# Optimization experiments

Measured on AMD Instinct MI355X. Metric: run time of the kernel, lower is better.

The kernel has to match this reference:

```python
import jax, jax.numpy as jnp
import numpy as np

N = 10000      # nodes
E = 160000     # edges (avg degree 16)
IN = 128       # in_channels
OUT = 64       # out_channels per head
H = 5          # heads


def setup_inputs() -> dict:
    key = jax.random.key(0)
    ks = jax.random.split(key, 20)

    def lin_w(k, fi, fo):
        return jax.random.normal(k, (fi, fo), jnp.float32) / np.float32(np.sqrt(fi))

    def lin_b(k, fo):
        return jax.random.normal(k, (fo,), jnp.float32) * 0.01

    return {
        "x": jax.random.normal(ks[0], (N, IN), jnp.float32),
        "edge_index": jax.random.randint(ks[1], (2, E), 0, N, dtype=jnp.int32),
        # layer 1 (in=IN)
        "q1_w": lin_w(ks[2], IN, H * OUT), "q1_b": lin_b(ks[3], H * OUT),
        "k1_w": lin_w(ks[4], IN, H * OUT), "k1_b": lin_b(ks[5], H * OUT),
        "v1_w": lin_w(ks[6], IN, H * OUT), "v1_b": lin_b(ks[7], H * OUT),
        "s1_w": lin_w(ks[8], IN, OUT),     "s1_b": lin_b(ks[9], OUT),
        # layer 2 (in=OUT)
        "q2_w": lin_w(ks[10], OUT, H * OUT), "q2_b": lin_b(ks[11], H * OUT),
        "k2_w": lin_w(ks[12], OUT, H * OUT), "k2_b": lin_b(ks[13], H * OUT),
        "v2_w": lin_w(ks[14], OUT, H * OUT), "v2_b": lin_b(ks[15], H * OUT),
        "s2_w": lin_w(ks[16], OUT, OUT),     "s2_b": lin_b(ks[17], OUT),
    }


def _transformer_conv(x, src, dst, qw, qb, kw, kb, vw, vb, sw, sb):
    """PyG TransformerConv: heads=H, concat=False (head mean), root_weight=True."""
    n = x.shape[0]
    q = (x @ qw + qb).reshape(n, H, OUT)
    k = (x @ kw + kb).reshape(n, H, OUT)
    v = (x @ vw + vb).reshape(n, H, OUT)
    # per-edge attention logits [E, H]
    alpha = jnp.einsum('ehc,ehc->eh', q[dst], k[src]) / jnp.sqrt(jnp.float32(OUT))
    # segment softmax over incoming edges of each destination node
    amax = jax.ops.segment_max(alpha, dst, num_segments=n)
    ex = jnp.exp(alpha - amax[dst])
    den = jax.ops.segment_sum(ex, dst, num_segments=n)
    a = ex / den[dst]
    # weighted scatter-add of source values -> [N, H, OUT]
    out = jax.ops.segment_sum(a[:, :, None] * v[src], dst, num_segments=n)
    return out.mean(axis=1) + x @ sw + sb  # concat=False mean + root skip


def reference(x, edge_index, q1_w, q1_b, k1_w, k1_b, v1_w, v1_b, s1_w, s1_b,
              q2_w, q2_b, k2_w, k2_b, v2_w, v2_b, s2_w, s2_b):
    src, dst = edge_index[0], edge_index[1]
    h = _transformer_conv(x, src, dst, q1_w, q1_b, k1_w, k1_b, v1_w, v1_b, s1_w, s1_b)
    h = jax.nn.relu(h)
    h = _transformer_conv(h, src, dst, q2_w, q2_b, k2_w, k2_b, v2_w, v2_b, s2_w, s2_b)
    return jax.nn.relu(h)
```

## Files before the change

kernel.cpp:

```cpp
#include <hip/hip_runtime.h>
#include <hip/hip_bf16.h>

#define N_NODES 10000
#define N_EDGES 160000
#define IN_CH   128
#define OUT_CH  64
#define HEADS   5
#define HO      320
#define NN64    (N_NODES * 64)
#define KVROW   320
#define SLOT_CAP 64

typedef __bf16 bf16;
typedef __bf16 bf16x4 __attribute__((ext_vector_type(4)));
typedef __bf16 bf16x8 __attribute__((ext_vector_type(8)));
typedef float  f32x4  __attribute__((ext_vector_type(4)));
typedef unsigned u32;

__device__ inline float bflo(u32 u) { return __builtin_bit_cast(float, u << 16); }
__device__ inline float bfhi(u32 u) { return __builtin_bit_cast(float, u & 0xffff0000u); }

__device__ inline void repack_one(const float* __restrict__ w, bf16* __restrict__ p,
                                  int i, int K, int NC) {
    int j    = i & 7;
    int lane = (i >> 3) & 63;
    int unit = i >> 9;
    int nkc  = K >> 5;
    int kc   = unit % nkc;
    int ctg  = unit / nkc;
    int col  = ctg * 16 + (lane & 15);
    int k    = kc * 32 + (lane >> 4) * 8 + j;
    p[i] = (bf16)w[(size_t)k * NC + col];
}

__global__ __launch_bounds__(256) void repack_weights(
    const float* q1, const float* k1, const float* v1, const float* s1,
    const float* q2, const float* k2, const float* v2, const float* s2,
    bf16* pq1, bf16* pk1, bf16* pv1, bf16* ps1,
    bf16* pq2, bf16* pk2, bf16* pv2, bf16* ps2,
    const float* __restrict__ x, bf16* __restrict__ xb, int* __restrict__ counts)
{
    int t = blockIdx.x * 256 + threadIdx.x;
    if (t < 196608) {
        if      (t <  40960) repack_one(q1, pq1, t,           128, 320);
        else if (t <  81920) repack_one(k1, pk1, t -  40960,  128, 320);
        else if (t < 122880) repack_one(v1, pv1, t -  81920,  128, 320);
        else if (t < 131072) repack_one(s1, ps1, t - 122880,  128,  64);
        else if (t < 151552) repack_one(q2, pq2, t - 131072,   64, 320);
        else if (t < 172032) repack_one(k2, pk2, t - 151552,   64, 320);
        else if (t < 192512) repack_one(v2, pv2, t - 172032,   64, 320);
        else                 repack_one(s2, ps2, t - 192512,   64,  64);
    } else if (t < 516608) {
        int i = t - 196608;
        f32x4 v = *reinterpret_cast<const f32x4*>(x + (size_t)4 * i);
        bf16x4 o;
        #pragma unroll
        for (int j = 0; j < 4; j++) o[j] = (bf16)v[j];
        *reinterpret_cast<bf16x4*>(xb + (size_t)4 * i) = o;
    } else if (t < 526608) {
        counts[t - 516608] = 0;
    }
}

template<int K, bool APPEND>
__global__ __launch_bounds__(256) void gemm_fused(
    const bf16* __restrict__ A, int M,
    const bf16* __restrict__ pq, const bf16* __restrict__ pk,
    const bf16* __restrict__ pv, const bf16* __restrict__ ps,
    const float* __restrict__ Bq, const float* __restrict__ Bk,
    const float* __restrict__ Bv, const float* __restrict__ Bs,
    u32* __restrict__ qp, bf16* __restrict__ q4,
    u32* __restrict__ kv, float* __restrict__ sout,
    const int* __restrict__ esrc, const int* __restrict__ edst,
    int* __restrict__ counts, int* __restrict__ slots)
{
    constexpr int NKC = K / 32;
    int gb = blockIdx.y;

    if constexpr (APPEND) {
        if (gb == 4) {
            const int stride = 157 * 256;
            for (int i = blockIdx.x * 256 + threadIdx.x; i < N_EDGES; i += stride) {
                int d = edst[i];
                int pos = atomicAdd(&counts[d], 1);
                if (pos < SLOT_CAP) slots[d * SLOT_CAP + pos] = esrc[i] * KVROW;
            }
            return;
        }
    }

    int lane = threadIdx.x & 63;
    int wv   = threadIdx.x >> 6;
    int lr = lane & 15, lg = lane >> 4;
    int rw0 = blockIdx.x * 64 + wv * 16;

    bf16x8 afrag[NKC];
    {
        int arow = rw0 + lr; if (arow > M - 1) arow = M - 1;
        const bf16* ap = A + (size_t)arow * K + lg * 8;
        #pragma unroll
        for (int kc = 0; kc < NKC; kc++)
            afrag[kc] = *reinterpret_cast<const bf16x8*>(ap + kc * 32);
    }

    if (gb < 3) {
        const bf16*  P  = (gb == 0) ? pq : (gb == 1) ? pk : pv;
        const float* Bb = (gb == 0) ? Bq : (gb == 1) ? Bk : Bv;
        #pragma unroll
        for (int ph = 0; ph < 2; ph++) {
            f32x4 acc0[4] = {}; f32x4 acc1[4] = {};
            #pragma unroll
            for (int ct = 0; ct < 4; ct++) {
                #pragma unroll
                for (int kc = 0; kc < NKC; kc++) {
                    bf16x8 b0 = *reinterpret_cast<const bf16x8*>(
                        P + ((size_t)((2 * ph + 0) * 4 + ct) * NKC + kc) * 512 + lane * 8);
                    bf16x8 b1 = *reinterpret_cast<const bf16x8*>(
                        P + ((size_t)((2 * ph + 1) * 4 + ct) * NKC + kc) * 512 + lane * 8);
                    acc0[ct] = __builtin_amdgcn_mfma_f32_16x16x32_bf16(afrag[kc], b0, acc0[ct], 0, 0, 0);
                    acc1[ct] = __builtin_amdgcn_mfma_f32_16x16x32_bf16(afrag[kc], b1, acc1[ct], 0, 0, 0);
                }
            }
            #pragma unroll
            for (int ct = 0; ct < 4; ct++) {
                int chan = ct * 16 + lr;
                float b0 = Bb[(2 * ph + 0) * 64 + chan];
                float b1 = Bb[(2 * ph + 1) * 64 + chan];
                #pragma unroll
                for (int r = 0; r < 4; r++) {
                    int row = rw0 + lg * 4 + r;
                    if (row >= M) continue;
                    u32 lo = __builtin_bit_cast(unsigned short, (bf16)(acc0[ct][r] + b0));
                    u32 hi = __builtin_bit_cast(unsigned short, (bf16)(acc1[ct][r] + b1));
                    u32 val = lo | (hi << 16);
                    if (gb == 0) qp[(size_t)ph * NN64 + (size_t)row * 64 + chan] = val;
                    else {
                        int rbase = (gb == 1) ? ph * 64 : 128 + ph * 64;
                        kv[(size_t)row * KVROW + rbase + chan] = val;
                    }
                }
            }
        }
    } else {
        bf16* kvb = (bf16*)kv;
        #pragma unroll
        for (int su = 0; su < 4; su++) {
            const bf16*  P  = (su == 0) ? pq : (su == 1) ? pk : (su == 2) ? pv : ps;
            const float* Bb = (su == 0) ? Bq : (su == 1) ? Bk : (su == 2) ? Bv : Bs;
            int ctg0 = (su < 3) ? 16 : 0;
            f32x4 acc[4] = {};
            #pragma unroll
            for (int ct = 0; ct < 4; ct++) {
                #pragma unroll
                for (int kc = 0; kc < NKC; kc++) {
                    bf16x8 b = *reinterpret_cast<const bf16x8*>(
                        P + ((size_t)(ctg0 + ct) * NKC + kc) * 512 + lane * 8);
                    acc[ct] = __builtin_amdgcn_mfma_f32_16x16x32_bf16(afrag[kc], b, acc[ct], 0, 0, 0);
                }
            }
            #pragma unroll
            for (int ct = 0; ct < 4; ct++) {
                int chan = ct * 16 + lr;
                float bb = (su < 3) ? Bb[256 + chan] : Bb[chan];
                #pragma unroll
                for (int r = 0; r < 4; r++) {
                    int row = rw0 + lg * 4 + r;
                    if (row >= M) continue;
                    float val = acc[ct][r] + bb;
                    if      (su == 0) q4[(size_t)row * 64 + chan] = (bf16)val;
                    else if (su == 1) kvb[(size_t)row * (2 * KVROW) + 512 + (chan >> 2) * 8 + (chan & 3)] = (bf16)val;
                    else if (su == 2) kvb[(size_t)row * (2 * KVROW) + 512 + (chan >> 2) * 8 + 4 + (chan & 3)] = (bf16)val;
                    else              sout[(size_t)row * 64 + chan] = val;
                }
            }
        }
    }
}


__device__ inline void load_qr(const u32* __restrict__ qp, const u32* __restrict__ q432,
                               int wid, int lr, f32x4 (&qr)[5])
{
    const float SC = 0.125f * 1.44269504089f;
    uint4 qA = *reinterpret_cast<const uint4*>(qp + (size_t)wid * 64 + 4 * lr);
    uint4 qB = *reinterpret_cast<const uint4*>(qp + NN64 + (size_t)wid * 64 + 4 * lr);
    uint2 qC = *reinterpret_cast<const uint2*>(q432 + (size_t)wid * 32 + 2 * lr);
    qr[0] = f32x4{bflo(qA.x), bflo(qA.y), bflo(qA.z), bflo(qA.w)} * SC;
    qr[1] = f32x4{bfhi(qA.x), bfhi(qA.y), bfhi(qA.z), bfhi(qA.w)} * SC;
    qr[2] = f32x4{bflo(qB.x), bflo(qB.y), bflo(qB.z), bflo(qB.w)} * SC;
    qr[3] = f32x4{bfhi(qB.x), bfhi(qB.y), bfhi(qB.z), bfhi(qB.w)} * SC;
    qr[4] = f32x4{bflo(qC.x), bfhi(qC.x), bflo(qC.y), bfhi(qC.y)} * SC;
}

__device__ inline void edge_accum(const u32* __restrict__ kv, int co, int lr, bool valid,
                                  const f32x4 (&qr)[5], float (&den)[5], f32x4 (&ac)[5])
{
    const u32* pa = kv + co + 4 * lr;
    uint4 kA = *reinterpret_cast<const uint4*>(pa);
    uint4 kB = *reinterpret_cast<const uint4*>(pa + 64);
    uint4 vA = *reinterpret_cast<const uint4*>(pa + 128);
    uint4 vB = *reinterpret_cast<const uint4*>(pa + 192);
    uint4 C  = *reinterpret_cast<const uint4*>(pa + 256);

    float t0 = qr[0][0]*bflo(kA.x) + qr[0][1]*bflo(kA.y) + qr[0][2]*bflo(kA.z) + qr[0][3]*bflo(kA.w);
    float t1 = qr[1][0]*bfhi(kA.x) + qr[1][1]*bfhi(kA.y) + qr[1][2]*bfhi(kA.z) + qr[1][3]*bfhi(kA.w);
    float t2 = qr[2][0]*bflo(kB.x) + qr[2][1]*bflo(kB.y) + qr[2][2]*bflo(kB.z) + qr[2][3]*bflo(kB.w);
    float t3 = qr[3][0]*bfhi(kB.x) + qr[3][1]*bfhi(kB.y) + qr[3][2]*bfhi(kB.z) + qr[3][3]*bfhi(kB.w);
    float t4 = qr[4][0]*bflo(C.x)  + qr[4][1]*bfhi(C.x)  + qr[4][2]*bflo(C.y)  + qr[4][3]*bfhi(C.y);

    #pragma unroll
    for (int m = 1; m <= 8; m <<= 1) {
        t0 += __shfl_xor(t0, m, 64);
        t1 += __shfl_xor(t1, m, 64);
        t2 += __shfl_xor(t2, m, 64);
        t3 += __shfl_xor(t3, m, 64);
        t4 += __shfl_xor(t4, m, 64);
    }
    float p0 = valid ? exp2f(t0) : 0.f;
    float p1 = valid ? exp2f(t1) : 0.f;
    float p2 = valid ? exp2f(t2) : 0.f;
    float p3 = valid ? exp2f(t3) : 0.f;
    float p4 = valid ? exp2f(t4) : 0.f;
    den[0] += p0; den[1] += p1; den[2] += p2; den[3] += p3; den[4] += p4;

    ac[0][0] += p0*bflo(vA.x); ac[0][1] += p0*bflo(vA.y); ac[0][2] += p0*bflo(vA.z); ac[0][3] += p0*bflo(vA.w);
    ac[1][0] += p1*bfhi(vA.x); ac[1][1] += p1*bfhi(vA.y); ac[1][2] += p1*bfhi(vA.z); ac[1][3] += p1*bfhi(vA.w);
    ac[2][0] += p2*bflo(vB.x); ac[2][1] += p2*bflo(vB.y); ac[2][2] += p2*bflo(vB.z); ac[2][3] += p2*bflo(vB.w);
    ac[3][0] += p3*bfhi(vB.x); ac[3][1] += p3*bfhi(vB.y); ac[3][2] += p3*bfhi(vB.z); ac[3][3] += p3*bfhi(vB.w);
    ac[4][0] += p4*bflo(C.z);  ac[4][1] += p4*bfhi(C.z);  ac[4][2] += p4*bflo(C.w);  ac[4][3] += p4*bfhi(C.w);
}

template<typename OT>
__global__ __launch_bounds__(256) void attn1w(
    const u32* __restrict__ qp, const bf16* __restrict__ q4,
    const u32* __restrict__ kv,
    const float* __restrict__ s, const int* __restrict__ counts,
    const int* __restrict__ slots, OT* __restrict__ out, int n)
{
    int wid  = blockIdx.x * 4 + (threadIdx.x >> 6);
    int lane = threadIdx.x & 63;
    if (wid >= n) return;
    int lr  = lane & 15;
    int qtr = lane >> 4;

    f32x4 qr[5];
    load_qr(qp, (const u32*)q4, wid, lr, qr);

    float den[5] = {};
    f32x4 ac[5] = {};

    int cnt = counts[wid];
    int deg = cnt < SLOT_CAP ? cnt : SLOT_CAP;
    if (deg > 0) {
        int myco = slots[(size_t)wid * SLOT_CAP + ((lane < deg) ? lane : 0)];
        int niter = (deg + 3) >> 2;
        for (int i = 0; i < niter; i++) {
            int slot  = i * 4 + qtr;
            bool valid = slot < deg;
            int co = __shfl(myco, valid ? slot : 0, 64);
            edge_accum(kv, co, lr, valid, qr, den, ac);
        }
    }

    #pragma unroll
    for (int m = 16; m <= 32; m <<= 1) {
        #pragma unroll
        for (int h = 0; h < 5; h++) {
            den[h] += __shfl_xor(den[h], m, 64);
            #pragma unroll
            for (int j = 0; j < 4; j++) ac[h][j] += __shfl_xor(ac[h][j], m, 64);
        }
    }

    if (qtr == 0) {
        float inv[5];
        #pragma unroll
        for (int h = 0; h < 5; h++) inv[h] = (den[h] > 0.f) ? 1.f / den[h] : 0.f;
        f32x4 sv = *reinterpret_cast<const f32x4*>(s + (size_t)wid * 64 + 4 * lr);
        f32x4 r;
        #pragma unroll
        for (int j = 0; j < 4; j++) {
            float sum = ac[0][j]*inv[0] + ac[1][j]*inv[1] + ac[2][j]*inv[2] + ac[3][j]*inv[3] + ac[4][j]*inv[4];
            r[j] = fmaxf(sum * 0.2f + sv[j], 0.f);
        }
        if constexpr (__is_same(OT, float)) {
            *reinterpret_cast<f32x4*>(out + (size_t)wid * 64 + 4 * lr) = r;
        } else {
            bf16x4 rb;
            #pragma unroll
            for (int j = 0; j < 4; j++) rb[j] = (bf16)r[j];
            *reinterpret_cast<bf16x4*>(out + (size_t)wid * 64 + 4 * lr) = rb;
        }
    }
}


extern "C" void kernel_launch(void* const* d_in, const int* in_sizes, int n_in,
                              void* d_out, int out_size, void* d_ws, size_t ws_size,
                              hipStream_t stream)
{
    const float* x   = (const float*)d_in[0];
    const int*   ei  = (const int*)d_in[1];
    const int*   src = ei;
    const int*   dst = ei + N_EDGES;
    const float* q1w = (const float*)d_in[2];  const float* q1b = (const float*)d_in[3];
    const float* k1w = (const float*)d_in[4];  const float* k1b = (const float*)d_in[5];
    const float* v1w = (const float*)d_in[6];  const float* v1b = (const float*)d_in[7];
    const float* s1w = (const float*)d_in[8];  const float* s1b = (const float*)d_in[9];
    const float* q2w = (const float*)d_in[10]; const float* q2b = (const float*)d_in[11];
    const float* k2w = (const float*)d_in[12]; const float* k2b = (const float*)d_in[13];
    const float* v2w = (const float*)d_in[14]; const float* v2b = (const float*)d_in[15];
    const float* s2w = (const float*)d_in[16]; const float* s2b = (const float*)d_in[17];

    char* ws = (char*)d_ws;
    size_t off = 0;
    auto alloc = [&](size_t bytes) -> void* {
        void* p = ws + off;
        off += (bytes + 255) & ~(size_t)255;
        return p;
    };
    u32*  qp   = (u32*) alloc((size_t)2 * NN64 * 4);
    bf16* q4   = (bf16*)alloc((size_t)NN64 * 2);
    u32*  kv   = (u32*) alloc((size_t)N_NODES * KVROW * 4);
    float* sbuf = (float*)alloc((size_t)NN64 * 4);
    bf16* xb   = (bf16*)alloc((size_t)N_NODES * IN_CH * 2);
    bf16* hb   = (bf16*)alloc((size_t)NN64 * 2);
    bf16* pq1 = (bf16*)alloc(40960 * 2);
    bf16* pk1 = (bf16*)alloc(40960 * 2);
    bf16* pv1 = (bf16*)alloc(40960 * 2);
    bf16* ps1 = (bf16*)alloc(8192 * 2);
    bf16* pq2 = (bf16*)alloc(20480 * 2);
    bf16* pk2 = (bf16*)alloc(20480 * 2);
    bf16* pv2 = (bf16*)alloc(20480 * 2);
    bf16* ps2 = (bf16*)alloc(4096 * 2);
    int*  counts = (int*)alloc((size_t)N_NODES * 4);
    int*  slots  = (int*)alloc((size_t)N_NODES * SLOT_CAP * 4);

    repack_weights<<<2058, 256, 0, stream>>>(q1w, k1w, v1w, s1w, q2w, k2w, v2w, s2w,
                                             pq1, pk1, pv1, ps1, pq2, pk2, pv2, ps2,
                                             x, xb, counts);

    dim3 g1((N_NODES + 63) / 64, 5);
    gemm_fused<IN_CH, true><<<g1, 256, 0, stream>>>(xb, N_NODES,
        pq1, pk1, pv1, ps1, q1b, k1b, v1b, s1b, qp, q4, kv, sbuf,
        src, dst, counts, slots);
    attn1w<bf16><<<(N_NODES + 3) / 4, 256, 0, stream>>>(
        qp, q4, kv, sbuf, counts, slots, hb, N_NODES);

    dim3 g2((N_NODES + 63) / 64, 4);
    gemm_fused<OUT_CH, false><<<g2, 256, 0, stream>>>(hb, N_NODES,
        pq2, pk2, pv2, ps2, q2b, k2b, v2b, s2b, qp, q4, kv, sbuf,
        src, dst, counts, slots);
    attn1w<float><<<(N_NODES + 3) / 4, 256, 0, stream>>>(
        qp, q4, kv, sbuf, counts, slots, (float*)d_out, N_NODES);
}
```

Measured before the change: 113.8 us.

## Split layer-1 attention by source-node partition for kv cache locality

Edges are bucketed per destination into four partitions by source-node range, and layer-1 attention runs as a partial pass per partition followed by a combine kernel that sums numerators and denominators. Grouping blocks by partition is meant to keep each pass's gathered K/V rows within a smaller working set that fits better in cache. The cost is an extra atomic bucketing pass, a bf16 partial buffer with extra writes and reads, and one more kernel launch. Dropping the per-node max is only safe as long as the logits stay small, and a cap of 24 edges per partition can drop edges. Storing the partial numerators in bf16 also loses precision.

```diff
diff --git a/kernel.cpp b/kernel.cpp
--- a/kernel.cpp
+++ b/kernel.cpp
@@ -10,15 +10,24 @@
 #define NN64    (N_NODES * 64)
 #define KVROW   320
 #define SLOT_CAP 64
+#define NPART   4
+#define PCAP    24
+#define PSTR    168
 
 typedef __bf16 bf16;
 typedef __bf16 bf16x4 __attribute__((ext_vector_type(4)));
 typedef __bf16 bf16x8 __attribute__((ext_vector_type(8)));
 typedef float  f32x4  __attribute__((ext_vector_type(4)));
 typedef unsigned u32;
+typedef unsigned short u16;
 
 __device__ inline float bflo(u32 u) { return __builtin_bit_cast(float, u << 16); }
 __device__ inline float bfhi(u32 u) { return __builtin_bit_cast(float, u & 0xffff0000u); }
+__device__ inline u32 pack2(float a, float b) {
+    u32 ua = __builtin_bit_cast(u16, (bf16)a);
+    u32 ub = __builtin_bit_cast(u16, (bf16)b);
+    return ua | (ub << 16);
+}
 
 __device__ inline void repack_one(const float* __restrict__ w, bf16* __restrict__ p,
                                   int i, int K, int NC) {
@@ -38,7 +47,8 @@
     const float* q2, const float* k2, const float* v2, const float* s2,
     bf16* pq1, bf16* pk1, bf16* pv1, bf16* ps1,
     bf16* pq2, bf16* pk2, bf16* pv2, bf16* ps2,
-    const float* __restrict__ x, bf16* __restrict__ xb, int* __restrict__ counts)
+    const float* __restrict__ x, bf16* __restrict__ xb,
+    int* __restrict__ counts, int* __restrict__ c2)
 {
     int t = blockIdx.x * 256 + threadIdx.x;
     if (t < 196608) {
@@ -59,6 +69,8 @@
         *reinterpret_cast<bf16x4*>(xb + (size_t)4 * i) = o;
     } else if (t < 526608) {
         counts[t - 516608] = 0;
+    } else if (t < 566608) {
+        c2[t - 526608] = 0;
     }
 }
 
@@ -72,7 +84,8 @@
     u32* __restrict__ qp, bf16* __restrict__ q4,
     u32* __restrict__ kv, float* __restrict__ sout,
     const int* __restrict__ esrc, const int* __restrict__ edst,
-    int* __restrict__ counts, int* __restrict__ slots)
+    int* __restrict__ counts, int* __restrict__ slots,
+    int* __restrict__ c2, int* __restrict__ slots2)
 {
     constexpr int NKC = K / 32;
     int gb = blockIdx.y;
@@ -82,8 +95,13 @@
             const int stride = 157 * 256;
             for (int i = blockIdx.x * 256 + threadIdx.x; i < N_EDGES; i += stride) {
                 int d = edst[i];
+                int s = esrc[i];
+                int co = s * KVROW;
                 int pos = atomicAdd(&counts[d], 1);
-                if (pos < SLOT_CAP) slots[d * SLOT_CAP + pos] = esrc[i] * KVROW;
+                if (pos < SLOT_CAP) slots[d * SLOT_CAP + pos] = co;
+                int p2 = s / 2500;
+                int pos2 = atomicAdd(&c2[d * NPART + p2], 1);
+                if (pos2 < PCAP) slots2[(d * NPART + p2) * PCAP + pos2] = co;
             }
             return;
         }
@@ -130,8 +148,8 @@
                 for (int r = 0; r < 4; r++) {
                     int row = rw0 + lg * 4 + r;
                     if (row >= M) continue;
-                    u32 lo = __builtin_bit_cast(unsigned short, (bf16)(acc0[ct][r] + b0));
-                    u32 hi = __builtin_bit_cast(unsigned short, (bf16)(acc1[ct][r] + b1));
+                    u32 lo = __builtin_bit_cast(u16, (bf16)(acc0[ct][r] + b0));
+                    u32 hi = __builtin_bit_cast(u16, (bf16)(acc1[ct][r] + b1));
                     u32 val = lo | (hi << 16);
                     if (gb == 0) qp[(size_t)ph * NN64 + (size_t)row * 64 + chan] = val;
                     else {
@@ -228,6 +246,84 @@
     ac[2][0] += p2*bflo(vB.x); ac[2][1] += p2*bflo(vB.y); ac[2][2] += p2*bflo(vB.z); ac[2][3] += p2*bflo(vB.w);
     ac[3][0] += p3*bfhi(vB.x); ac[3][1] += p3*bfhi(vB.y); ac[3][2] += p3*bfhi(vB.z); ac[3][3] += p3*bfhi(vB.w);
     ac[4][0] += p4*bflo(C.z);  ac[4][1] += p4*bfhi(C.z);  ac[4][2] += p4*bflo(C.w);  ac[4][3] += p4*bfhi(C.w);
+}
+
+__global__ __launch_bounds__(256) void attn_partA(
+    const u32* __restrict__ qp, const bf16* __restrict__ q4,
+    const u32* __restrict__ kv, const int* __restrict__ c2,
+    const int* __restrict__ slots2, u32* __restrict__ part, int n)
+{
+    int bid  = blockIdx.x;
+    int p    = bid & 3;
+    int wv   = threadIdx.x >> 6;
+    int node = (bid >> 2) * 4 + wv;
+    int lane = threadIdx.x & 63;
+    int lr = lane & 15, qtr = lane >> 4;
+
+    float den[5] = {};
+    f32x4 ac[5] = {};
+
+    int cnt = c2[node * NPART + p];
+    int deg = cnt < PCAP ? cnt : PCAP;
+    if (deg > 0) {
+        f32x4 qr[5];
+        load_qr(qp, (const u32*)q4, node, lr, qr);
+        int myco = slots2[(node * NPART + p) * PCAP + ((lane < deg) ? lane : 0)];
+        int niter = (deg + 3) >> 2;
+        for (int i = 0; i < niter; i++) {
+            int slot  = i * 4 + qtr;
+            bool valid = slot < deg;
+            int co = __shfl(myco, valid ? slot : 0, 64);
+            edge_accum(kv, co, lr, valid, qr, den, ac);
+        }
+        #pragma unroll
+        for (int m = 16; m <= 32; m <<= 1) {
+            #pragma unroll
+            for (int h = 0; h < 5; h++) {
+                den[h] += __shfl_xor(den[h], m, 64);
+                #pragma unroll
+                for (int j = 0; j < 4; j++) ac[h][j] += __shfl_xor(ac[h][j], m, 64);
+            }
+        }
+    }
+    u32* pb = part + ((size_t)p * n + (size_t)node) * PSTR;
+    if (qtr == 0) {
+        #pragma unroll
+        for (int h = 0; h < 5; h++) {
+            pb[h * 32 + lr * 2 + 0] = pack2(ac[h][0], ac[h][1]);
+            pb[h * 32 + lr * 2 + 1] = pack2(ac[h][2], ac[h][3]);
+        }
+        if (lr == 0) {
+            #pragma unroll
+            for (int h = 0; h < 5; h++)
+                reinterpret_cast<float*>(pb)[160 + h] = den[h];
+        }
+    }
+}
+
+template<typename OT>
+__global__ __launch_bounds__(256) void attn_partB(
+    const u32* __restrict__ part, const float* __restrict__ s,
+    OT* __restrict__ out, int n)
+{
+    int t = blockIdx.x * 256 + threadIdx.x;
+    int node = t >> 6, c = t & 63;
+    float den[5] = {}, acc[5] = {};
+    #pragma unroll
+    for (int p = 0; p < NPART; p++) {
+        const u32* pb = part + ((size_t)p * n + (size_t)node) * PSTR;
+        #pragma unroll
+        for (int h = 0; h < 5; h++) {
+            u32 v = pb[h * 32 + (c >> 2) * 2 + ((c & 3) >> 1)];
+            acc[h] += (c & 1) ? bfhi(v) : bflo(v);
+            den[h] += reinterpret_cast<const float*>(pb)[160 + h];
+        }
+    }
+    float r = 0.f;
+    #pragma unroll
+    for (int h = 0; h < 5; h++) r += (den[h] > 0.f) ? acc[h] / den[h] : 0.f;
+    r = fmaxf(r * 0.2f + s[t], 0.f);
+    out[t] = (OT)r;
 }
 
 template<typename OT>
@@ -335,22 +431,25 @@
     bf16* ps2 = (bf16*)alloc(4096 * 2);
     int*  counts = (int*)alloc((size_t)N_NODES * 4);
     int*  slots  = (int*)alloc((size_t)N_NODES * SLOT_CAP * 4);
-
-    repack_weights<<<2058, 256, 0, stream>>>(q1w, k1w, v1w, s1w, q2w, k2w, v2w, s2w,
+    int*  c2     = (int*)alloc((size_t)N_NODES * NPART * 4);
+    int*  slots2 = (int*)alloc((size_t)N_NODES * NPART * PCAP * 4);
+    u32*  part   = (u32*)alloc((size_t)NPART * N_NODES * PSTR * 4);
+
+    repack_weights<<<2214, 256, 0, stream>>>(q1w, k1w, v1w, s1w, q2w, k2w, v2w, s2w,
                                              pq1, pk1, pv1, ps1, pq2, pk2, pv2, ps2,
-                                             x, xb, counts);
+                                             x, xb, counts, c2);
 
     dim3 g1((N_NODES + 63) / 64, 5);
     gemm_fused<IN_CH, true><<<g1, 256, 0, stream>>>(xb, N_NODES,
         pq1, pk1, pv1, ps1, q1b, k1b, v1b, s1b, qp, q4, kv, sbuf,
-        src, dst, counts, slots);
-    attn1w<bf16><<<(N_NODES + 3) / 4, 256, 0, stream>>>(
-        qp, q4, kv, sbuf, counts, slots, hb, N_NODES);
+        src, dst, counts, slots, c2, slots2);
+    attn_partA<<<N_NODES, 256, 0, stream>>>(qp, q4, kv, c2, slots2, part, N_NODES);
+    attn_partB<bf16><<<(N_NODES * 64) / 256, 256, 0, stream>>>(part, sbuf, hb, N_NODES);
 
     dim3 g2((N_NODES + 63) / 64, 4);
     gemm_fused<OUT_CH, false><<<g2, 256, 0, stream>>>(hb, N_NODES,
         pq2, pk2, pv2, ps2, q2b, k2b, v2b, s2b, qp, q4, kv, sbuf,
-        src, dst, counts, slots);
+        src, dst, counts, slots, c2, slots2);
     attn1w<float><<<(N_NODES + 3) / 4, 256, 0, stream>>>(
         qp, q4, kv, sbuf, counts, slots, (float*)d_out, N_NODES);
 }
```

Result: slower. 136.0 us (+19.5%).
